# Performance work log

Measured on AMD Instinct MI355X. Metric: run time of the kernel, lower is better.

Reference implementation:

```python
import jax, jax.numpy as jnp
import numpy as np

HIDDEN = 2048
N_HEADS = 16
HEAD_DIM = HIDDEN // N_HEADS  # 128
BATCH = 2
SEQ = 2048


def setup_inputs() -> dict:
    key = jax.random.key(0)
    ks = jax.random.split(key, 9)
    std = HIDDEN ** -0.5
    inp = {
        "hidden_states": jax.random.normal(ks[0], (BATCH, SEQ, HIDDEN), dtype=jnp.float32),
        "q_w": jax.random.normal(ks[1], (HIDDEN, HIDDEN), dtype=jnp.float32) * std,
        "k_w": jax.random.normal(ks[2], (HIDDEN, HIDDEN), dtype=jnp.float32) * std,
        "v_w": jax.random.normal(ks[3], (HIDDEN, HIDDEN), dtype=jnp.float32) * std,
        "o_w": jax.random.normal(ks[4], (HIDDEN, HIDDEN), dtype=jnp.float32) * std,
        "q_b": jnp.zeros((HIDDEN,), dtype=jnp.float32),
        "k_b": jnp.zeros((HIDDEN,), dtype=jnp.float32),
        "v_b": jnp.zeros((HIDDEN,), dtype=jnp.float32),
        "o_b": jnp.zeros((HIDDEN,), dtype=jnp.float32),
    }
    return inp


def reference(hidden_states, q_w, k_w, v_w, o_w, q_b, k_b, v_b, o_b):
    b, s, _ = hidden_states.shape
    # Projections (nn.Linear applies x @ W^T + b); split heads -> [b, h, s, d]
    def proj(w, bias):
        y = hidden_states @ w.T + bias
        return y.reshape(b, s, N_HEADS, HEAD_DIM).transpose(0, 2, 1, 3)

    q = proj(q_w, q_b)
    k = proj(k_w, k_b)
    v = proj(v_w, v_b)

    scale = 1.0 / jnp.sqrt(jnp.float32(HEAD_DIM))
    scores = jnp.einsum("bhqd,bhkd->bhqk", q, k) * scale  # [b, h, s, s]

    # causal mask: mask positions where k > q (triu, diagonal=1)
    qi = jnp.arange(s)[:, None]
    ki = jnp.arange(s)[None, :]
    scores = jnp.where(ki > qi, -jnp.inf, scores)

    attn = jax.nn.softmax(scores.astype(jnp.float32), axis=-1).astype(q.dtype)
    out = jnp.einsum("bhqk,bhkd->bhqd", attn, v)
    out = out.transpose(0, 2, 1, 3).reshape(b, s, HIDDEN)
    return out @ o_w.T + o_b
```

## Files before the change

kernel.cpp:

```cpp
#include <hip/hip_runtime.h>

#define S_HID 2048
#define S_SEQ 2048
#define S_B   2
#define S_NH  16
#define S_HD  128
#define S_M   (S_B * S_SEQ)
#define S_BH  (S_B * S_NH)

typedef __bf16 bf16_t;
typedef __bf16 bf16x8 __attribute__((ext_vector_type(8)));
typedef __bf16 bf16x4 __attribute__((ext_vector_type(4)));
typedef float  floatx4 __attribute__((ext_vector_type(4)));
typedef float  floatx16 __attribute__((ext_vector_type(16)));

typedef __attribute__((address_space(1))) unsigned int as1_uint;
typedef __attribute__((address_space(3))) unsigned int as3_uint;

__device__ __forceinline__ void gload_lds16(const void* g, void* l) {
    __builtin_amdgcn_global_load_lds((as1_uint*)g, (as3_uint*)l, 16, 0, 0);
}

__global__ void cvt_bf16(const float* __restrict__ src, bf16_t* __restrict__ dst, int n) {
    int nv = n >> 2;
    int stride = gridDim.x * blockDim.x;
    for (int i = blockIdx.x * blockDim.x + threadIdx.x; i < nv; i += stride) {
        float4 v = ((const float4*)src)[i];
        bf16x4 o;
        o.x = (bf16_t)v.x; o.y = (bf16_t)v.y; o.z = (bf16_t)v.z; o.w = (bf16_t)v.w;
        ((bf16x4*)dst)[i] = o;
    }
}

__global__ __launch_bounds__(256, 2)
void gemm_bt(const bf16_t* __restrict__ A, const bf16_t* __restrict__ W,
             const float* __restrict__ bias, void* __restrict__ out,
             int mode, float scale) {
    __shared__ __align__(16) bf16_t ldsA[128 * 64];
    __shared__ __align__(16) bf16_t ldsB[128 * 64];
    const int tid = threadIdx.x;
    const int wid = tid >> 6, lane = tid & 63;
    const int m0 = blockIdx.y * 128, n0 = blockIdx.x * 128;
    const int wm = (wid & 1) * 64, wn = (wid >> 1) * 64;
    const int lm = lane & 15, quad = lane >> 4;
    const int srow = lane >> 3;
    const int scol = lane & 7;

    floatx4 acc[4][4];
    #pragma unroll
    for (int i = 0; i < 4; ++i)
        #pragma unroll
        for (int j = 0; j < 4; ++j)
            acc[i][j] = (floatx4){0.f, 0.f, 0.f, 0.f};

    for (int kt = 0; kt < S_HID; kt += 64) {
        #pragma unroll
        for (int i = 0; i < 4; ++i) {
            int slot = i * 4 + wid;
            int row = slot * 8 + srow;
            int cg = scol ^ (row & 7);
            gload_lds16(A + (size_t)(m0 + row) * S_HID + kt + cg * 8, &ldsA[slot * 512]);
            gload_lds16(W + (size_t)(n0 + row) * S_HID + kt + cg * 8, &ldsB[slot * 512]);
        }
        __syncthreads();
        #pragma unroll
        for (int k2 = 0; k2 < 2; ++k2) {
            bf16x8 af[4], bfr[4];
            #pragma unroll
            for (int i = 0; i < 4; ++i) {
                int row = wm + i * 16 + lm;
                int cc = (k2 * 4 + quad) ^ (row & 7);
                af[i] = *(const bf16x8*)&ldsA[row * 64 + cc * 8];
            }
            #pragma unroll
            for (int j = 0; j < 4; ++j) {
                int row = wn + j * 16 + lm;
                int cc = (k2 * 4 + quad) ^ (row & 7);
                bfr[j] = *(const bf16x8*)&ldsB[row * 64 + cc * 8];
            }
            #pragma unroll
            for (int i = 0; i < 4; ++i)
                #pragma unroll
                for (int j = 0; j < 4; ++j)
                    acc[i][j] = __builtin_amdgcn_mfma_f32_16x16x32_bf16(af[i], bfr[j], acc[i][j], 0, 0, 0);
        }
        __syncthreads();
    }

    if (mode == 0) {
        bf16_t* Ob = (bf16_t*)out;
        #pragma unroll
        for (int i = 0; i < 4; ++i) {
            #pragma unroll
            for (int j = 0; j < 4; ++j) {
                int n = n0 + wn + j * 16 + lm;
                float bv = bias[n];
                int h = n >> 7, d = n & 127;
                #pragma unroll
                for (int r = 0; r < 4; ++r) {
                    int m = m0 + wm + i * 16 + quad * 4 + r;
                    int b = m >> 11, s = m & 2047;
                    Ob[(((size_t)(b * S_NH + h)) * S_SEQ + s) * S_HD + d] =
                        (bf16_t)((acc[i][j][r] + bv) * scale);
                }
            }
        }
    } else if (mode == 1) {
        float* Of = (float*)out;
        #pragma unroll
        for (int i = 0; i < 4; ++i) {
            #pragma unroll
            for (int j = 0; j < 4; ++j) {
                int n = n0 + wn + j * 16 + lm;
                float bv = bias[n];
                #pragma unroll
                for (int r = 0; r < 4; ++r) {
                    int m = m0 + wm + i * 16 + quad * 4 + r;
                    Of[(size_t)m * S_HID + n] = acc[i][j][r] + bv;
                }
            }
        }
    } else {
        bf16_t* Vt = (bf16_t*)out;
        #pragma unroll
        for (int i = 0; i < 4; ++i) {
            #pragma unroll
            for (int j = 0; j < 4; ++j) {
                int n = n0 + wn + j * 16 + lm;
                float bv = bias[n];
                int h = n >> 7, d = n & 127;
                int m = m0 + wm + i * 16 + quad * 4;
                int b = m >> 11, s = m & 2047;
                bf16x4 ov;
                #pragma unroll
                for (int r = 0; r < 4; ++r) ov[r] = (bf16_t)(acc[i][j][r] + bv);
                *(bf16x4*)&Vt[(((size_t)(b * S_NH + h)) * S_HD + d) * S_SEQ + s] = ov;
            }
        }
    }
}

__device__ __forceinline__ bf16x8 make_pfrag(bf16x4 lo, bf16x4 hi, int h) {
    int2 li = __builtin_bit_cast(int2, lo);
    int2 hh = __builtin_bit_cast(int2, hi);
    int2 xl, xh;
    xl.x = __shfl_xor(li.x, 32); xl.y = __shfl_xor(li.y, 32);
    xh.x = __shfl_xor(hh.x, 32); xh.y = __shfl_xor(hh.y, 32);
    int2 flo, fhi;
    flo.x = h ? xh.x : li.x;  flo.y = h ? xh.y : li.y;
    fhi.x = h ? hh.x : xl.x;  fhi.y = h ? hh.y : xl.y;
    bf16x4 a = __builtin_bit_cast(bf16x4, flo);
    bf16x4 b = __builtin_bit_cast(bf16x4, fhi);
    return __builtin_shufflevector(a, b, 0, 1, 2, 3, 4, 5, 6, 7);
}

__global__ __launch_bounds__(256, 1)
void attn(const bf16_t* __restrict__ Q, const bf16_t* __restrict__ K,
          const bf16_t* __restrict__ Vt, bf16_t* __restrict__ O) {
    __shared__ __align__(16) bf16_t ldsK[2][128 * 128];
    __shared__ __align__(16) bf16_t ldsV[2][128 * 128];
    const int tid = threadIdx.x, wid = tid >> 6, lane = tid & 63;
    const int lm = lane & 15, quad = lane >> 4;
    const int c31 = lane & 31, h = lane >> 5, r7 = lane & 7;
    const int bx = blockIdx.x;
    const int bh = bx & 31, pair = bx >> 5;
    const int b = bh >> 4, hd = bh & 15;

    const bf16_t* Kbase = K + (size_t)bh * S_SEQ * S_HD;
    const bf16_t* Vbase = Vt + (size_t)bh * S_HD * S_SEQ;

    int pp = 0;
    #pragma unroll
    for (int seg = 0; seg < 2; ++seg) {
        const int q0 = seg ? (1920 - pair * 128) : (pair * 128);
        const int qcol = q0 + wid * 32 + c31;
        const int nkt = (q0 >> 7) + 1;

        bf16x8 qf[8];
        {
            const bf16_t* qp = Q + ((size_t)bh * S_SEQ + qcol) * S_HD + h * 8;
            #pragma unroll
            for (int ks = 0; ks < 8; ++ks) qf[ks] = *(const bf16x8*)(qp + ks * 16);
        }

        floatx16 oa[4];
        #pragma unroll
        for (int jd = 0; jd < 4; ++jd)
            #pragma unroll
            for (int e = 0; e < 16; ++e) oa[jd][e] = 0.f;
        float m_st = -1e30f, l_st = 0.f;

        {
            #pragma unroll
            for (int i = 0; i < 8; ++i) {
                int slot = i * 4 + wid;
                int row = slot * 4 + quad;
                int cg = lm ^ (row & 7);
                gload_lds16(Kbase + (size_t)row * S_HD + cg * 8, &ldsK[pp][slot * 512]);
                gload_lds16(Vbase + (size_t)row * S_SEQ + cg * 8, &ldsV[pp][slot * 512]);
            }
        }

        for (int kti = 0; kti < nkt; ++kti) {
            const int kt = kti * 128;
            __syncthreads();

            if (kti + 1 < nkt) {
                const int ktn = kt + 128;
                #pragma unroll
                for (int i = 0; i < 8; ++i) {
                    int slot = i * 4 + wid;
                    int row = slot * 4 + quad;
                    int cg = lm ^ (row & 7);
                    gload_lds16(Kbase + (size_t)(ktn + row) * S_HD + cg * 8, &ldsK[pp ^ 1][slot * 512]);
                    gload_lds16(Vbase + (size_t)row * S_SEQ + ktn + cg * 8, &ldsV[pp ^ 1][slot * 512]);
                }
            }

            floatx16 sa[4];
            #pragma unroll
            for (int jr = 0; jr < 4; ++jr)
                #pragma unroll
                for (int e = 0; e < 16; ++e) sa[jr][e] = 0.f;
            #pragma unroll
            for (int ks = 0; ks < 8; ++ks) {
                #pragma unroll
                for (int jr = 0; jr < 4; ++jr) {
                    int row = jr * 32 + c31;
                    bf16x8 kf = *(const bf16x8*)&ldsK[pp][row * 128 + (((ks * 2 + h) ^ r7)) * 8];
                    sa[jr] = __builtin_amdgcn_mfma_f32_32x32x16_bf16(kf, qf[ks], sa[jr], 0, 0, 0);
                }
            }

            if (kti == nkt - 1) {
                #pragma unroll
                for (int jr = 0; jr < 4; ++jr)
                    #pragma unroll
                    for (int rr = 0; rr < 16; ++rr) {
                        int key = kt + jr * 32 + (rr & 3) + 8 * (rr >> 2) + 4 * h;
                        if (key > qcol) sa[jr][rr] = -1e30f;
                    }
            }

            float mx = -1e30f;
            #pragma unroll
            for (int jr = 0; jr < 4; ++jr)
                #pragma unroll
                for (int rr = 0; rr < 16; ++rr) mx = fmaxf(mx, sa[jr][rr]);
            mx = fmaxf(mx, __shfl_xor(mx, 32));
            float mn = fmaxf(m_st, mx);
            float al = __builtin_amdgcn_exp2f(m_st - mn);
            m_st = mn;

            float rs = 0.f;
            bf16x8 pf[8];
            #pragma unroll
            for (int jr = 0; jr < 4; ++jr) {
                bf16x4 pk[4];
                #pragma unroll
                for (int g = 0; g < 4; ++g)
                    #pragma unroll
                    for (int e = 0; e < 4; ++e) {
                        float p = __builtin_amdgcn_exp2f(sa[jr][g * 4 + e] - mn);
                        rs += p;
                        pk[g][e] = (bf16_t)p;
                    }
                pf[jr * 2]     = make_pfrag(pk[0], pk[1], h);
                pf[jr * 2 + 1] = make_pfrag(pk[2], pk[3], h);
            }
            rs += __shfl_xor(rs, 32);
            l_st = l_st * al + rs;
            #pragma unroll
            for (int jd = 0; jd < 4; ++jd)
                #pragma unroll
                for (int e = 0; e < 16; ++e) oa[jd][e] *= al;

            #pragma unroll
            for (int kb = 0; kb < 8; ++kb) {
                #pragma unroll
                for (int jd = 0; jd < 4; ++jd) {
                    int row = jd * 32 + c31;
                    bf16x8 vf = *(const bf16x8*)&ldsV[pp][row * 128 + (((kb * 2 + h) ^ r7)) * 8];
                    oa[jd] = __builtin_amdgcn_mfma_f32_32x32x16_bf16(vf, pf[kb], oa[jd], 0, 0, 0);
                }
            }
            pp ^= 1;
        }

        float inv = 1.0f / l_st;
        bf16_t* op = O + ((size_t)b * S_SEQ + qcol) * S_HID + hd * S_HD;
        #pragma unroll
        for (int jd = 0; jd < 4; ++jd)
            #pragma unroll
            for (int g = 0; g < 4; ++g) {
                bf16x4 ov;
                #pragma unroll
                for (int e = 0; e < 4; ++e) ov[e] = (bf16_t)(oa[jd][g * 4 + e] * inv);
                *(bf16x4*)&op[jd * 32 + g * 8 + 4 * h] = ov;
            }
    }
}

extern "C" void kernel_launch(void* const* d_in, const int* in_sizes, int n_in,
                              void* d_out, int out_size, void* d_ws, size_t ws_size,
                              hipStream_t stream) {
    const float* hs = (const float*)d_in[0];
    const float* qw = (const float*)d_in[1];
    const float* kw = (const float*)d_in[2];
    const float* vw = (const float*)d_in[3];
    const float* ow = (const float*)d_in[4];
    const float* qbias = (const float*)d_in[5];
    const float* kbias = (const float*)d_in[6];
    const float* vbias = (const float*)d_in[7];
    const float* obias = (const float*)d_in[8];

    char* ws = (char*)d_ws;
    bf16_t* Xb  = (bf16_t*)(ws + 0);
    bf16_t* Wqb = (bf16_t*)(ws + 16777216);
    bf16_t* Wkb = (bf16_t*)(ws + 25165824);
    bf16_t* Wvb = (bf16_t*)(ws + 33554432);
    bf16_t* Wob = (bf16_t*)(ws + 41943040);
    bf16_t* Qb  = (bf16_t*)(ws + 50331648);
    bf16_t* Kb  = (bf16_t*)(ws + 67108864);
    bf16_t* Vtb = (bf16_t*)(ws + 83886080);
    bf16_t* Ob  = Xb;

    cvt_bf16<<<1024, 256, 0, stream>>>(hs, Xb, S_M * S_HID);
    cvt_bf16<<<512, 256, 0, stream>>>(qw, Wqb, S_HID * S_HID);
    cvt_bf16<<<512, 256, 0, stream>>>(kw, Wkb, S_HID * S_HID);
    cvt_bf16<<<512, 256, 0, stream>>>(vw, Wvb, S_HID * S_HID);
    cvt_bf16<<<512, 256, 0, stream>>>(ow, Wob, S_HID * S_HID);

    dim3 gg(S_HID / 128, S_M / 128);
    const float qscale = 0.08838834764831845f * 1.4426950408889634f;
    gemm_bt<<<gg, 256, 0, stream>>>(Xb, Wqb, qbias, (void*)Qb, 0, qscale);
    gemm_bt<<<gg, 256, 0, stream>>>(Xb, Wkb, kbias, (void*)Kb, 0, 1.0f);
    gemm_bt<<<gg, 256, 0, stream>>>(Xb, Wvb, vbias, (void*)Vtb, 2, 1.0f);

    attn<<<256, 256, 0, stream>>>(Qb, Kb, Vtb, Ob);

    gemm_bt<<<gg, 256, 0, stream>>>(Ob, Wob, obias, d_out, 1, 1.0f);
}
```

Baseline: 380.7 us.

## Fuse QKV projections into one GEMM launch and merge weight conversions

```diff
diff --git a/kernel.cpp b/kernel.cpp
--- a/kernel.cpp
+++ b/kernel.cpp
@@ -32,10 +32,29 @@
     }
 }
 
-__global__ __launch_bounds__(256, 2)
-void gemm_bt(const bf16_t* __restrict__ A, const bf16_t* __restrict__ W,
-             const float* __restrict__ bias, void* __restrict__ out,
-             int mode, float scale) {
+__global__ void cvt_w4(const float* __restrict__ q, const float* __restrict__ k,
+                       const float* __restrict__ v, const float* __restrict__ o,
+                       bf16_t* __restrict__ dst) {
+    const int per = (S_HID * S_HID) >> 2;
+    const int total = per * 4;
+    int stride = gridDim.x * blockDim.x;
+    for (int i = blockIdx.x * blockDim.x + threadIdx.x; i < total; i += stride) {
+        int region = i >> 20;
+        int local = i & (per - 1);
+        const float* src = region == 0 ? q : region == 1 ? k : region == 2 ? v : o;
+        float4 x = ((const float4*)src)[local];
+        bf16x4 y;
+        y.x = (bf16_t)x.x; y.y = (bf16_t)x.y; y.z = (bf16_t)x.z; y.w = (bf16_t)x.w;
+        ((bf16x4*)dst)[i] = y;
+    }
+}
+
+__global__ __launch_bounds__(256, 3)
+void gemm_qkv(const bf16_t* __restrict__ A, const bf16_t* __restrict__ W,
+              const float* __restrict__ qbias, const float* __restrict__ kbias,
+              const float* __restrict__ vbias,
+              bf16_t* __restrict__ Qo, bf16_t* __restrict__ Ko, bf16_t* __restrict__ Vto,
+              float qscale) {
     __shared__ __align__(16) bf16_t ldsA[128 * 64];
     __shared__ __align__(16) bf16_t ldsB[128 * 64];
     const int tid = threadIdx.x;
@@ -87,15 +106,19 @@
         __syncthreads();
     }
 
-    if (mode == 0) {
-        bf16_t* Ob = (bf16_t*)out;
+    const int region = n0 >> 11;
+    if (region < 2) {
+        bf16_t* Ob = region ? Ko : Qo;
+        const float* bias = region ? kbias : qbias;
+        float scale = region ? 1.0f : qscale;
         #pragma unroll
         for (int i = 0; i < 4; ++i) {
             #pragma unroll
             for (int j = 0; j < 4; ++j) {
                 int n = n0 + wn + j * 16 + lm;
-                float bv = bias[n];
-                int h = n >> 7, d = n & 127;
+                float bv = bias[n & 2047];
+                int nl = n & 2047;
+                int h = nl >> 7, d = nl & 127;
                 #pragma unroll
                 for (int r = 0; r < 4; ++r) {
                     int m = m0 + wm + i * 16 + quad * 4 + r;
@@ -105,36 +128,90 @@
                 }
             }
         }
-    } else if (mode == 1) {
-        float* Of = (float*)out;
+    } else {
         #pragma unroll
         for (int i = 0; i < 4; ++i) {
             #pragma unroll
             for (int j = 0; j < 4; ++j) {
                 int n = n0 + wn + j * 16 + lm;
-                float bv = bias[n];
-                #pragma unroll
-                for (int r = 0; r < 4; ++r) {
-                    int m = m0 + wm + i * 16 + quad * 4 + r;
-                    Of[(size_t)m * S_HID + n] = acc[i][j][r] + bv;
-                }
-            }
-        }
-    } else {
-        bf16_t* Vt = (bf16_t*)out;
-        #pragma unroll
-        for (int i = 0; i < 4; ++i) {
-            #pragma unroll
-            for (int j = 0; j < 4; ++j) {
-                int n = n0 + wn + j * 16 + lm;
-                float bv = bias[n];
-                int h = n >> 7, d = n & 127;
+                int nl = n & 2047;
+                float bv = vbias[nl];
+                int h = nl >> 7, d = nl & 127;
                 int m = m0 + wm + i * 16 + quad * 4;
                 int b = m >> 11, s = m & 2047;
                 bf16x4 ov;
                 #pragma unroll
                 for (int r = 0; r < 4; ++r) ov[r] = (bf16_t)(acc[i][j][r] + bv);
-                *(bf16x4*)&Vt[(((size_t)(b * S_NH + h)) * S_HD + d) * S_SEQ + s] = ov;
+                *(bf16x4*)&Vto[(((size_t)(b * S_NH + h)) * S_HD + d) * S_SEQ + s] = ov;
+            }
+        }
+    }
+}
+
+__global__ __launch_bounds__(256, 3)
+void gemm_out(const bf16_t* __restrict__ A, const bf16_t* __restrict__ W,
+              const float* __restrict__ bias, float* __restrict__ out) {
+    __shared__ __align__(16) bf16_t ldsA[128 * 64];
+    __shared__ __align__(16) bf16_t ldsB[128 * 64];
+    const int tid = threadIdx.x;
+    const int wid = tid >> 6, lane = tid & 63;
+    const int m0 = blockIdx.y * 128, n0 = blockIdx.x * 128;
+    const int wm = (wid & 1) * 64, wn = (wid >> 1) * 64;
+    const int lm = lane & 15, quad = lane >> 4;
+    const int srow = lane >> 3;
+    const int scol = lane & 7;
+
+    floatx4 acc[4][4];
+    #pragma unroll
+    for (int i = 0; i < 4; ++i)
+        #pragma unroll
+        for (int j = 0; j < 4; ++j)
+            acc[i][j] = (floatx4){0.f, 0.f, 0.f, 0.f};
+
+    for (int kt = 0; kt < S_HID; kt += 64) {
+        #pragma unroll
+        for (int i = 0; i < 4; ++i) {
+            int slot = i * 4 + wid;
+            int row = slot * 8 + srow;
+            int cg = scol ^ (row & 7);
+            gload_lds16(A + (size_t)(m0 + row) * S_HID + kt + cg * 8, &ldsA[slot * 512]);
+            gload_lds16(W + (size_t)(n0 + row) * S_HID + kt + cg * 8, &ldsB[slot * 512]);
+        }
+        __syncthreads();
+        #pragma unroll
+        for (int k2 = 0; k2 < 2; ++k2) {
+            bf16x8 af[4], bfr[4];
+            #pragma unroll
+            for (int i = 0; i < 4; ++i) {
+                int row = wm + i * 16 + lm;
+                int cc = (k2 * 4 + quad) ^ (row & 7);
+                af[i] = *(const bf16x8*)&ldsA[row * 64 + cc * 8];
+            }
+            #pragma unroll
+            for (int j = 0; j < 4; ++j) {
+                int row = wn + j * 16 + lm;
+                int cc = (k2 * 4 + quad) ^ (row & 7);
+                bfr[j] = *(const bf16x8*)&ldsB[row * 64 + cc * 8];
+            }
+            #pragma unroll
+            for (int i = 0; i < 4; ++i)
+                #pragma unroll
+                for (int j = 0; j < 4; ++j)
+                    acc[i][j] = __builtin_amdgcn_mfma_f32_16x16x32_bf16(af[i], bfr[j], acc[i][j], 0, 0, 0);
+        }
+        __syncthreads();
+    }
+
+    #pragma unroll
+    for (int i = 0; i < 4; ++i) {
+        #pragma unroll
+        for (int j = 0; j < 4; ++j) {
+            int n = n0 + wn + j * 16 + lm;
+            float bv = bias[n];
+            #pragma unroll
+            for (int r = 0; r < 4; ++r) {
+                int m = m0 + wm + i * 16 + quad * 4 + r;
+                out[(size_t)m * S_HID + n] = acc[i][j][r] + bv;
             }
         }
     }
@@ -315,29 +392,22 @@
     const float* obias = (const float*)d_in[8];
 
     char* ws = (char*)d_ws;
-    bf16_t* Xb  = (bf16_t*)(ws + 0);
-    bf16_t* Wqb = (bf16_t*)(ws + 16777216);
-    bf16_t* Wkb = (bf16_t*)(ws + 25165824);
-    bf16_t* Wvb = (bf16_t*)(ws + 33554432);
-    bf16_t* Wob = (bf16_t*)(ws + 41943040);
-    bf16_t* Qb  = (bf16_t*)(ws + 50331648);
-    bf16_t* Kb  = (bf16_t*)(ws + 67108864);
-    bf16_t* Vtb = (bf16_t*)(ws + 83886080);
-    bf16_t* Ob  = Xb;
+    bf16_t* Xb   = (bf16_t*)(ws + 0);
+    bf16_t* Wqkv = (bf16_t*)(ws + 16777216);
+    bf16_t* Wob  = (bf16_t*)(ws + 41943040);
+    bf16_t* Qb   = (bf16_t*)(ws + 50331648);
+    bf16_t* Kb   = (bf16_t*)(ws + 67108864);
+    bf16_t* Vtb  = (bf16_t*)(ws + 83886080);
+    bf16_t* Ob   = Xb;
 
     cvt_bf16<<<1024, 256, 0, stream>>>(hs, Xb, S_M * S_HID);
-    cvt_bf16<<<512, 256, 0, stream>>>(qw, Wqb, S_HID * S_HID);
-    cvt_bf16<<<512, 256, 0, stream>>>(kw, Wkb, S_HID * S_HID);
-    cvt_bf16<<<512, 256, 0, stream>>>(vw, Wvb, S_HID * S_HID);
-    cvt_bf16<<<512, 256, 0, stream>>>(ow, Wob, S_HID * S_HID);
-
-    dim3 gg(S_HID / 128, S_M / 128);
+    cvt_w4<<<1024, 256, 0, stream>>>(qw, kw, vw, ow, Wqkv);
+
     const float qscale = 0.08838834764831845f * 1.4426950408889634f;
-    gemm_bt<<<gg, 256, 0, stream>>>(Xb, Wqb, qbias, (void*)Qb, 0, qscale);
-    gemm_bt<<<gg, 256, 0, stream>>>(Xb, Wkb, kbias, (void*)Kb, 0, 1.0f);
-    gemm_bt<<<gg, 256, 0, stream>>>(Xb, Wvb, vbias, (void*)Vtb, 2, 1.0f);
+    gemm_qkv<<<dim3(48, 32), 256, 0, stream>>>(Xb, Wqkv, qbias, kbias, vbias,
+                                               Qb, Kb, Vtb, qscale);
 
     attn<<<256, 256, 0, stream>>>(Qb, Kb, Vtb, Ob);
 
-    gemm_bt<<<gg, 256, 0, stream>>>(Ob, Wob, obias, d_out, 1, 1.0f);
-}
+    gemm_out<<<dim3(16, 32), 256, 0, stream>>>(Ob, Wob, obias, (float*)d_out);
+}
```

New measurement: 364.4 us. 1.04x faster.
